# Performance work log

Measured on AMD Instinct MI355X. Metric: run time of the kernel, lower is better.

## Reference

```python
import jax, jax.numpy as jnp
import numpy as np

TOP_K = 2
LORA_SCALE = 32.0 / 16.0  # alpha / rank


def setup_inputs() -> dict:
    key = jax.random.key(0)
    ks = jax.random.split(key, 11)
    N, D, F, E, R = 1024, 2048, 5632, 8, 16
    s = lambda k, shape, fan: jax.random.normal(k, shape, jnp.float32) / np.sqrt(fan)
    return {
        "x": jax.random.normal(ks[0], (N, D), jnp.float32),
        "gate_w": s(ks[1], (E, D), D),
        "W1": s(ks[2], (F, D), D),
        "W3": s(ks[3], (F, D), D),
        "W2": s(ks[4], (D, F), F),
        "A1": s(ks[5], (E, R, D), D),
        "B1": s(ks[6], (F, R), R)[None].repeat(E, 0) * 0.0 + s(ks[6], (E, F, R), R),
        "A3": s(ks[7], (E, R, D), D),
        "B3": s(ks[8], (E, F, R), R),
        "A2": s(ks[9], (E, R, F), F),
        "B2": s(ks[10], (E, D, R), R),
    }


def reference(x, gate_w, W1, W3, W2, A1, B1, A3, B3, A2, B2):
    # --- router: softmax over experts, top-k, renormalized combine weights ---
    logits = x @ gate_w.T                                   # [N, E]
    probs = jax.nn.softmax(logits, axis=-1)
    topw, topi = jax.lax.top_k(probs, TOP_K)                # [N, K]
    topw = topw / jnp.sum(topw, axis=-1, keepdims=True)
    E = gate_w.shape[0]
    w = jnp.sum(jax.nn.one_hot(topi, E, dtype=x.dtype) * topw[..., None], axis=1)  # [N, E]

    # --- experts: shared base weights + per-expert LoRA (fused SwiGLU) ---
    base1 = x @ W1.T                                        # [N, F]
    base3 = x @ W3.T                                        # [N, F]
    l1 = jnp.einsum("nd,erd->ner", x, A1)                   # rank-R bottleneck
    l3 = jnp.einsum("nd,erd->ner", x, A3)
    h1 = base1[:, None, :] + LORA_SCALE * jnp.einsum("ner,efr->nef", l1, B1)  # [N, E, F]
    h3 = base3[:, None, :] + LORA_SCALE * jnp.einsum("ner,efr->nef", l3, B3)
    s = jax.nn.silu(h1) * h3                                # [N, E, F]

    # down-projection: shared W2 applied to the routed mixture, plus per-expert LoRA
    s_mix = jnp.einsum("ne,nef->nf", w, s)                  # [N, F]
    out = s_mix @ W2.T                                      # [N, D]
    l2 = jnp.einsum("nef,erf->ner", s, A2) * (w[:, :, None] * LORA_SCALE)
    out = out + jnp.einsum("ner,edr->nd", l2, B2)           # [N, D]
    return out, logits
```

## Files before the change

kernel.cpp:

```cpp
#include <hip/hip_runtime.h>

typedef unsigned int u32;
typedef unsigned short u16;

#define N_TOK 1024
#define D_DIM 2048
#define F_DIM 5632
#define E_NUM 8
#define R_DIM 16
#define LSCALE 2.0f
#define FT 256
#define NT (F_DIM / FT)
#define TC 8
#define BN13 11520
#define ZSPLIT 8

typedef __bf16 bf16x8 __attribute__((ext_vector_type(8)));
typedef float f32x4 __attribute__((ext_vector_type(4)));
typedef u16 u16x8 __attribute__((ext_vector_type(8)));

__device__ inline u16 f2bf(float f) {
    u32 u = __builtin_bit_cast(u32, f);
    u32 r = (u + 0x7fffu + ((u >> 16) & 1u)) >> 16;
    return (u16)r;
}
__device__ inline float bf2f(u16 h) {
    u32 u = ((u32)h) << 16;
    return __builtin_bit_cast(float, u);
}

#define LGKM0() do { asm volatile("s_waitcnt lgkmcnt(0)" ::: "memory"); \
                     __builtin_amdgcn_sched_barrier(0); } while (0)
#define VMC(n)  do { asm volatile("s_waitcnt vmcnt(" #n ")" ::: "memory"); \
                     __builtin_amdgcn_sched_barrier(0); } while (0)

__global__ __launch_bounds__(256) void cvt_all(const float* __restrict__ x,
                                               const float* __restrict__ W1,
                                               const float* __restrict__ W3,
                                               const float* __restrict__ A1,
                                               const float* __restrict__ A3,
                                               const float* __restrict__ W2,
                                               const float* __restrict__ B1,
                                               const float* __restrict__ B3,
                                               u16* __restrict__ xb,
                                               u16* __restrict__ w13,
                                               u16* __restrict__ w2b,
                                               u16* __restrict__ b1b,
                                               u16* __restrict__ b3b) {
    int i = blockIdx.x * 256 + threadIdx.x;
    const float* src;
    u16* dst;
    int off;
    if (i < 524288)       { src = x;  dst = xb;             off = i; }
    else if (i < 3407872) { src = W1; dst = w13;            off = i - 524288; }
    else if (i < 6291456) { src = W3; dst = w13 + 11534336; off = i - 3407872; }
    else if (i < 6356992) { src = A1; dst = w13 + 23068672; off = i - 6291456; }
    else if (i < 6422528) { src = A3; dst = w13 + 23330816; off = i - 6356992; }
    else if (i < 9306112) { src = W2; dst = w2b;            off = i - 6422528; }
    else if (i < 9486336) { src = B1; dst = b1b;            off = i - 9306112; }
    else                  { src = B3; dst = b3b;            off = i - 9486336; }
    float4 v = ((const float4*)src)[off];
    union { u16 h[4]; ushort4 u4; } o;
    o.h[0] = f2bf(v.x); o.h[1] = f2bf(v.y); o.h[2] = f2bf(v.z); o.h[3] = f2bf(v.w);
    ((ushort4*)dst)[off] = o.u4;
}

__global__ __launch_bounds__(256) void a2_transpose(const float* __restrict__ A2,
                                                    u16* __restrict__ A2t) {
    int e = blockIdx.y;
    int f = blockIdx.x * 256 + threadIdx.x;
    u16 row[16];
#pragma unroll
    for (int r = 0; r < 16; ++r)
        row[r] = f2bf(A2[((size_t)e * R_DIM + r) * F_DIM + f]);
    u16* dst = A2t + ((size_t)e * F_DIM + f) * 16;
#pragma unroll
    for (int q = 0; q < 2; ++q)
        ((ulonglong2*)dst)[q] = ((ulonglong2*)row)[q];
}

__global__ __launch_bounds__(256) void router_kernel(const float* __restrict__ x,
                                                     const float* __restrict__ gw,
                                                     float* __restrict__ logits,
                                                     int* __restrict__ ridx,
                                                     float* __restrict__ rw) {
    int n = blockIdx.x;
    int tid = threadIdx.x;
    float part[E_NUM];
#pragma unroll
    for (int e = 0; e < E_NUM; ++e) part[e] = 0.f;
    const float* xr = x + (size_t)n * D_DIM;
    for (int d = tid; d < D_DIM; d += 256) {
        float xv = xr[d];
#pragma unroll
        for (int e = 0; e < E_NUM; ++e) part[e] += xv * gw[e * D_DIM + d];
    }
    __shared__ float sh[E_NUM][256];
#pragma unroll
    for (int e = 0; e < E_NUM; ++e) sh[e][tid] = part[e];
    __syncthreads();
    for (int off = 128; off > 0; off >>= 1) {
        if (tid < off) {
#pragma unroll
            for (int e = 0; e < E_NUM; ++e) sh[e][tid] += sh[e][tid + off];
        }
        __syncthreads();
    }
    if (tid == 0) {
        float lg[E_NUM], p[E_NUM];
        float mx = -1e30f;
        for (int e = 0; e < E_NUM; ++e) {
            lg[e] = sh[e][0];
            logits[n * E_NUM + e] = lg[e];
            if (lg[e] > mx) mx = lg[e];
        }
        float s = 0.f;
        for (int e = 0; e < E_NUM; ++e) { p[e] = expf(lg[e] - mx); s += p[e]; }
        for (int e = 0; e < E_NUM; ++e) p[e] /= s;
        int i1 = 0;
        for (int e = 1; e < E_NUM; ++e) if (p[e] > p[i1]) i1 = e;
        int i2 = (i1 == 0) ? 1 : 0;
        for (int e = 0; e < E_NUM; ++e) if (e != i1 && p[e] > p[i2]) i2 = e;
        float t = p[i1] + p[i2];
        ridx[n * 2] = i1; ridx[n * 2 + 1] = i2;
        rw[n * 2] = p[i1] / t; rw[n * 2 + 1] = p[i2] / t;
    }
}

__global__ __launch_bounds__(64) void zero_counts(int* counts) {
    if (threadIdx.x < E_NUM) counts[threadIdx.x] = 0;
}
__global__ __launch_bounds__(256) void build_lists(const int* __restrict__ ridx,
                                                   int* __restrict__ counts,
                                                   u32* __restrict__ lists) {
    int n = blockIdx.x * 256 + threadIdx.x;
    if (n >= N_TOK) return;
#pragma unroll
    for (int k = 0; k < 2; ++k) {
        int e = ridx[n * 2 + k];
        int slot = atomicAdd(&counts[e], 1);
        lists[e * N_TOK + slot] = (u32)n | ((u32)k << 16);
    }
}

__global__ __launch_bounds__(512, 2) void gemm256(const u16* __restrict__ A,
                                                  const u16* __restrict__ B,
                                                  float* __restrict__ C,
                                                  int N, int K, int kslice,
                                                  int mode, int ntm, int ntn) {
    __shared__ __align__(16) u16 lds[2][2][2][256 * 32];

    const int nb = gridDim.x;
    const int fb = blockIdx.x;
    const int qq = nb >> 3, rr = nb & 7;
    const int xcd = fb & 7, lo = fb >> 3;
    const int wg = (xcd < rr ? xcd * (qq + 1) : rr * (qq + 1) + (xcd - rr) * qq) + lo;

    const int mt = wg % ntm;
    const int t2 = wg / ntm;
    const int nt = t2 % ntn;
    const int zt = t2 / ntn;

    const int bm0 = mt * 256;
    const int bn0 = nt * 256;
    const int kb = zt * kslice;

    const int tid = threadIdx.x;
    const int lane = tid & 63;
    const int wave = tid >> 6;
    const int quad = lane >> 4;
    const int l16 = lane & 15;
    const int swz = (l16 & 8) << 1;
    const int wm = (wave >> 2) * 128;
    const int wn = (wave & 3) * 64;

    f32x4 zero = {0.f, 0.f, 0.f, 0.f};
    f32x4 acc[8][4];
#pragma unroll
    for (int i = 0; i < 8; ++i)
#pragma unroll
        for (int j = 0; j < 4; ++j) acc[i][j] = zero;

    auto stageHalf = [&](const u16* __restrict__ G, int mat, int buf, int h,
                         int k0, int rowBase) {
#pragma unroll
        for (int j = 0; j < 2; ++j) {
            int seg = wave * 2 + j;
            int plane = seg >> 3;
            int rb = seg & 7;
            int r = h * 128 + rb * 16 + (lane >> 2);
            int slot = lane & 3;
            int gcol = k0 + plane * 32 + ((slot * 8) ^ ((r & 8) << 1));
            const u16* gp = G + (size_t)(rowBase + r) * K + gcol;
            u16* lp = &lds[mat][buf][plane][(h * 128 + rb * 16) * 32] + lane * 8;
            __builtin_amdgcn_global_load_lds((const __attribute__((address_space(1))) u32*)gp,
                                             (__attribute__((address_space(3))) u32*)lp,
                                             16, 0, 0);
        }
    };

    const int nk = kslice >> 6;

    stageHalf(A, 0, 0, 0, kb, bm0);
    stageHalf(A, 0, 0, 1, kb, bm0);
    stageHalf(B, 1, 0, 0, kb, bn0);
    stageHalf(B, 1, 0, 1, kb, bn0);
    stageHalf(A, 0, 1, 0, kb + 64, bm0);
    stageHalf(A, 0, 1, 1, kb + 64, bm0);
    VMC(4);
    __builtin_amdgcn_s_barrier();

    bf16x8 af[8][2];
    for (int t = 0; t < nk; ++t) {
        const int buf = t & 1;
        const int k0 = kb + t * 64;

        {
            bf16x8 bf[2][2];
#pragma unroll
            for (int mi = 0; mi < 4; ++mi)
#pragma unroll
                for (int ks = 0; ks < 2; ++ks)
                    af[mi][ks] = *(const bf16x8*)&lds[0][buf][ks]
                        [(wm + mi * 16 + l16) * 32 + ((quad * 8) ^ swz)];
#pragma unroll
            for (int ni = 0; ni < 2; ++ni)
#pragma unroll
                for (int ks = 0; ks < 2; ++ks)
                    bf[ni][ks] = *(const bf16x8*)&lds[1][buf][ks]
                        [(wn + ni * 16 + l16) * 32 + ((quad * 8) ^ swz)];
            if (t + 1 < nk) stageHalf(B, 1, buf ^ 1, 0, k0 + 64, bn0);
            __builtin_amdgcn_s_barrier();
            LGKM0();
            __builtin_amdgcn_s_setprio(1);
#pragma unroll
            for (int mi = 0; mi < 4; ++mi)
#pragma unroll
                for (int ni = 0; ni < 2; ++ni)
#pragma unroll
                    for (int ks = 0; ks < 2; ++ks)
                        acc[mi][ni] = __builtin_amdgcn_mfma_f32_16x16x32_bf16(
                            af[mi][ks], bf[ni][ks], acc[mi][ni], 0, 0, 0);
            __builtin_amdgcn_s_setprio(0);
            __builtin_amdgcn_s_barrier();
        }

        {
            bf16x8 bf[2][2];
#pragma unroll
            for (int mi = 0; mi < 4; ++mi)
#pragma unroll
                for (int ks = 0; ks < 2; ++ks)
                    af[4 + mi][ks] = *(const bf16x8*)&lds[0][buf][ks]
                        [(wm + (4 + mi) * 16 + l16) * 32 + ((quad * 8) ^ swz)];
#pragma unroll
            for (int ni = 0; ni < 2; ++ni)
#pragma unroll
                for (int ks = 0; ks < 2; ++ks)
                    bf[ni][ks] = *(const bf16x8*)&lds[1][buf][ks]
                        [(wn + (2 + ni) * 16 + l16) * 32 + ((quad * 8) ^ swz)];
            if (t + 1 < nk) stageHalf(B, 1, buf ^ 1, 1, k0 + 64, bn0);
            __builtin_amdgcn_s_barrier();
            LGKM0();
            __builtin_amdgcn_s_setprio(1);
#pragma unroll
            for (int mi = 0; mi < 4; ++mi)
#pragma unroll
                for (int ni = 0; ni < 2; ++ni)
#pragma unroll
                    for (int ks = 0; ks < 2; ++ks)
                        acc[mi][2 + ni] = __builtin_amdgcn_mfma_f32_16x16x32_bf16(
                            af[mi][ks], bf[ni][ks], acc[mi][2 + ni], 0, 0, 0);
            __builtin_amdgcn_s_setprio(0);
            __builtin_amdgcn_s_barrier();

            if (t + 2 < nk) stageHalf(A, 0, buf, 0, k0 + 128, bm0);
            __builtin_amdgcn_s_barrier();
            __builtin_amdgcn_s_setprio(1);
#pragma unroll
            for (int mi = 0; mi < 4; ++mi)
#pragma unroll
                for (int ni = 0; ni < 2; ++ni)
#pragma unroll
                    for (int ks = 0; ks < 2; ++ks)
                        acc[4 + mi][2 + ni] = __builtin_amdgcn_mfma_f32_16x16x32_bf16(
                            af[4 + mi][ks], bf[ni][ks], acc[4 + mi][2 + ni], 0, 0, 0);
            __builtin_amdgcn_s_setprio(0);
            __builtin_amdgcn_s_barrier();
        }

        {
            bf16x8 bf[2][2];
#pragma unroll
            for (int ni = 0; ni < 2; ++ni)
#pragma unroll
                for (int ks = 0; ks < 2; ++ks)
                    bf[ni][ks] = *(const bf16x8*)&lds[1][buf][ks]
                        [(wn + ni * 16 + l16) * 32 + ((quad * 8) ^ swz)];
            if (t + 2 < nk) stageHalf(A, 0, buf, 1, k0 + 128, bm0);
            __builtin_amdgcn_s_barrier();
            LGKM0();
            __builtin_amdgcn_s_setprio(1);
#pragma unroll
            for (int mi = 0; mi < 4; ++mi)
#pragma unroll
                for (int ni = 0; ni < 2; ++ni)
#pragma unroll
                    for (int ks = 0; ks < 2; ++ks)
                        acc[4 + mi][ni] = __builtin_amdgcn_mfma_f32_16x16x32_bf16(
                            af[4 + mi][ks], bf[ni][ks], acc[4 + mi][ni], 0, 0, 0);
            __builtin_amdgcn_s_setprio(0);
            if (t < nk - 2)       { VMC(4); }
            else if (t == nk - 2) { VMC(0); }
            __builtin_amdgcn_s_barrier();
        }
    }

    float* Cz = C + (size_t)zt * ntm * 256 * N;
#pragma unroll
    for (int mi = 0; mi < 8; ++mi)
#pragma unroll
        for (int ni = 0; ni < 4; ++ni) {
            int col = bn0 + wn + ni * 16 + l16;
#pragma unroll
            for (int i = 0; i < 4; ++i) {
                int row = bm0 + wm + mi * 16 + quad * 4 + i;
                if (mode == 1) {
                    ((u16*)C)[(size_t)row * N + col] = f2bf(acc[mi][ni][i]);
                } else {
                    Cz[(size_t)row * N + col] = acc[mi][ni][i];
                }
            }
        }
}

__global__ __launch_bounds__(256) void act_v2b(const u16* __restrict__ base13,
                                               const u16* __restrict__ B1b,
                                               const u16* __restrict__ B3b,
                                               const u32* __restrict__ lists,
                                               const int* __restrict__ counts,
                                               const float* __restrict__ rw,
                                               u16* __restrict__ sbuf) {
    const int ft = blockIdx.x;
    const int e  = blockIdx.y;
    const int z  = blockIdx.z;
    const int tid = threadIdx.x;
    const int lane = tid & 63;
    const int wave = tid >> 6;
    const int f_lane = ft * FT + lane * 4;

    u16x8 w1c[8], w3c[8];
    {
        const u16* p1 = B1b + ((size_t)e * F_DIM + f_lane) * 16;
        const u16* p3 = B3b + ((size_t)e * F_DIM + f_lane) * 16;
#pragma unroll
        for (int c = 0; c < 8; ++c) {
            w1c[c] = *(const u16x8*)(p1 + c * 8);
            w3c[c] = *(const u16x8*)(p3 + c * 8);
        }
    }

    const int T = counts[e];
    for (int i = z * 4 + wave; i < T; i += TC * 4) {
        u32 ent = lists[e * N_TOK + i];
        int n = (int)(ent & 0xFFFFu);
        int k = (int)(ent >> 16);
        float wt = rw[n * 2 + k];

        float la1[16], la3[16];
        {
            const u16x8* pl1 = (const u16x8*)(base13 + (size_t)n * BN13 + 11264 + e * 16);
            const u16x8* pl3 = (const u16x8*)(base13 + (size_t)n * BN13 + 11392 + e * 16);
#pragma unroll
            for (int h = 0; h < 2; ++h) {
                u16x8 t1 = pl1[h], t3 = pl3[h];
#pragma unroll
                for (int qq = 0; qq < 8; ++qq) {
                    la1[h * 8 + qq] = LSCALE * bf2f(t1[qq]);
                    la3[h * 8 + qq] = LSCALE * bf2f(t3[qq]);
                }
            }
        }

        ushort4 b1u = *(const ushort4*)(base13 + (size_t)n * BN13 + f_lane);
        ushort4 b3u = *(const ushort4*)(base13 + (size_t)n * BN13 + 5632 + f_lane);
        const u16* b1p = (const u16*)&b1u;
        const u16* b3p = (const u16*)&b3u;

        u16 sv[4];
#pragma unroll
        for (int j = 0; j < 4; ++j) {
            float h1 = bf2f(b1p[j]);
            float h3 = bf2f(b3p[j]);
#pragma unroll
            for (int qq = 0; qq < 8; ++qq) {
                h1 += la1[qq] * bf2f(w1c[2 * j][qq]);
                h3 += la3[qq] * bf2f(w3c[2 * j][qq]);
            }
#pragma unroll
            for (int qq = 0; qq < 8; ++qq) {
                h1 += la1[8 + qq] * bf2f(w1c[2 * j + 1][qq]);
                h3 += la3[8 + qq] * bf2f(w3c[2 * j + 1][qq]);
            }
            float sg = h1 / (1.f + __expf(-h1));
            sv[j] = f2bf(wt * sg * h3);
        }
        *(ushort4*)(sbuf + ((size_t)k * N_TOK + n) * F_DIM + f_lane) = *(ushort4*)sv;
    }
}

__global__ __launch_bounds__(256) void combine_kernel(const u16* __restrict__ sbuf,
                                                      u16* __restrict__ smix) {
    size_t i = ((size_t)blockIdx.x * 256 + threadIdx.x) * 8;
    u16x8 a = *(const u16x8*)(sbuf + i);
    u16x8 b = *(const u16x8*)(sbuf + (size_t)N_TOK * F_DIM + i);
    u16x8 o;
#pragma unroll
    for (int q = 0; q < 8; ++q) o[q] = f2bf(bf2f(a[q]) + bf2f(b[q]));
    *(u16x8*)(smix + i) = o;
}

__global__ __launch_bounds__(256) void lora_down_v4(const u16* __restrict__ sbuf,
                                                    const u16* __restrict__ A2t,
                                                    const int* __restrict__ ridx,
                                                    const float* __restrict__ B2,
                                                    const float* __restrict__ pbuf,
                                                    float* __restrict__ out) {
    const int n = blockIdx.x, tid = threadIdx.x;
    __shared__ float part[2][32][16];
    __shared__ float fin[2][16];
    __shared__ int se[2];
    if (tid < 2) se[tid] = ridx[n * 2 + tid];
    __syncthreads();

    {
        const int k = tid >> 7;
        const int tt = tid & 127;
        const int rq = tt & 3;
        const int fc = tt >> 2;
        const int e = se[k];
        const u16* srow = sbuf + ((size_t)k * N_TOK + n) * F_DIM + fc * 176;
        const u16* arow = A2t + ((size_t)e * F_DIM + fc * 176) * 16 + rq * 4;
        float acc0 = 0.f, acc1 = 0.f, acc2 = 0.f, acc3 = 0.f;
#pragma unroll 4
        for (int f = 0; f < 176; ++f) {
            float sv = bf2f(srow[f]);
            ushort4 wr = *(const ushort4*)(arow + (size_t)f * 16);
            acc0 += sv * bf2f(wr.x);
            acc1 += sv * bf2f(wr.y);
            acc2 += sv * bf2f(wr.z);
            acc3 += sv * bf2f(wr.w);
        }
        part[k][fc][rq * 4 + 0] = acc0;
        part[k][fc][rq * 4 + 1] = acc1;
        part[k][fc][rq * 4 + 2] = acc2;
        part[k][fc][rq * 4 + 3] = acc3;
    }
    __syncthreads();
    if (tid < 32) {
        int k = tid >> 4, r = tid & 15;
        float s = 0.f;
#pragma unroll
        for (int fc = 0; fc < 32; ++fc) s += part[k][fc][r];
        fin[k][r] = LSCALE * s;
    }
    __syncthreads();

    float a0[16], a1v[16];
#pragma unroll
    for (int r = 0; r < 16; ++r) { a0[r] = fin[0][r]; a1v[r] = fin[1][r]; }
    const float* B2a = B2 + (size_t)se[0] * D_DIM * R_DIM;
    const float* B2b = B2 + (size_t)se[1] * D_DIM * R_DIM;
    const float* prow = pbuf + (size_t)n * D_DIM;
    float* orow = out + (size_t)n * D_DIM;
    for (int d = tid; d < D_DIM; d += 256) {
        const float4* pa = (const float4*)(B2a + (size_t)d * 16);
        const float4* pb = (const float4*)(B2b + (size_t)d * 16);
        float acc = 0.f;
#pragma unroll
        for (int q = 0; q < 4; ++q) {
            float4 va = pa[q];
            acc += a0[q * 4] * va.x + a0[q * 4 + 1] * va.y +
                   a0[q * 4 + 2] * va.z + a0[q * 4 + 3] * va.w;
            float4 vb = pb[q];
            acc += a1v[q * 4] * vb.x + a1v[q * 4 + 1] * vb.y +
                   a1v[q * 4 + 2] * vb.z + a1v[q * 4 + 3] * vb.w;
        }
        float ps = 0.f;
#pragma unroll
        for (int z = 0; z < ZSPLIT; ++z)
            ps += prow[(size_t)z * N_TOK * D_DIM + d];
        orow[d] = acc + ps;
    }
}

extern "C" void kernel_launch(void* const* d_in, const int* in_sizes, int n_in,
                              void* d_out, int out_size, void* d_ws, size_t ws_size,
                              hipStream_t stream) {
    const float* x  = (const float*)d_in[0];
    const float* gw = (const float*)d_in[1];
    const float* W1 = (const float*)d_in[2];
    const float* W3 = (const float*)d_in[3];
    const float* W2 = (const float*)d_in[4];
    const float* A1 = (const float*)d_in[5];
    const float* B1 = (const float*)d_in[6];
    const float* A3 = (const float*)d_in[7];
    const float* B3 = (const float*)d_in[8];
    const float* A2 = (const float*)d_in[9];
    const float* B2 = (const float*)d_in[10];
    float* out = (float*)d_out;
    float* logits = out + (size_t)N_TOK * D_DIM;

    char* ws = (char*)d_ws;
    size_t off = 0;
    auto alloc = [&](size_t bytes) { char* p = ws + off; off += (bytes + 255) & ~(size_t)255; return p; };
    u16*   xb    = (u16*)alloc((size_t)N_TOK * D_DIM * 2);
    u16*   W13b  = (u16*)alloc((size_t)BN13 * D_DIM * 2);
    u16*   W2b   = (u16*)alloc((size_t)D_DIM * F_DIM * 2);
    u16*   base13= (u16*)alloc((size_t)N_TOK * BN13 * 2);
    int*   ridx  = (int*)alloc((size_t)N_TOK * 2 * 4);
    float* rwt   = (float*)alloc((size_t)N_TOK * 2 * 4);
    u16*   B1b   = (u16*)alloc((size_t)E_NUM * F_DIM * R_DIM * 2);
    u16*   B3b   = (u16*)alloc((size_t)E_NUM * F_DIM * R_DIM * 2);
    u16*   A2t   = (u16*)alloc((size_t)E_NUM * F_DIM * R_DIM * 2);
    int*   counts= (int*)alloc(64);
    u32*   lists = (u32*)alloc((size_t)E_NUM * N_TOK * 4);
    u16*   sbuf  = (u16*)alloc((size_t)2 * N_TOK * F_DIM * 2);
    u16*   smixb = (u16*)alloc((size_t)N_TOK * F_DIM * 2);
    float* pbuf  = (float*)alloc((size_t)ZSPLIT * N_TOK * D_DIM * 4);
    (void)ws_size; (void)in_sizes; (void)n_in; (void)out_size;

    cvt_all<<<37760, 256, 0, stream>>>(x, W1, W3, A1, A3, W2, B1, B3,
                                       xb, W13b, W2b, B1b, B3b);
    a2_transpose<<<dim3(F_DIM / 256, E_NUM), 256, 0, stream>>>(A2, A2t);

    router_kernel<<<N_TOK, 256, 0, stream>>>(x, gw, logits, ridx, rwt);
    zero_counts<<<1, 64, 0, stream>>>(counts);
    build_lists<<<N_TOK / 256, 256, 0, stream>>>(ridx, counts, lists);

    gemm256<<<180, 512, 0, stream>>>(xb, W13b, (float*)base13,
                                     BN13, D_DIM, D_DIM, 1, 4, 45);

    act_v2b<<<dim3(NT, E_NUM, TC), 256, 0, stream>>>(base13, B1b, B3b,
                                                     lists, counts, rwt, sbuf);

    combine_kernel<<<(N_TOK * F_DIM / 8) / 256, 256, 0, stream>>>(sbuf, smixb);

    gemm256<<<256, 512, 0, stream>>>(smixb, W2b, pbuf,
                                     D_DIM, F_DIM, 704, 0, 4, 8);

    lora_down_v4<<<N_TOK, 256, 0, stream>>>(sbuf, A2t, ridx, B2, pbuf, out);
}
```

Before: 404.5 us.

## Restructure GEMM main loop into four k-split phases with B prefetched two ahead

Reorganizes the inner MFMA loop of the tiled GEMM from three phases (mixed quadrants, both k-halves) into four phases. Each phase covers half of the M rows and one 32-wide k-slice against all N columns. The staging schedule is swapped so B is double-buffered two tiles ahead and A one tile ahead. Register footprint drops because fragments are held per k-slice (4 A + 8 B vectors) instead of af[8][2]. Each phase now issues 16 MFMAs with a barrier between phases, and the prefetch ordering and barrier placement change how global-to-LDS loads overlap with compute.

```diff
diff --git a/kernel.cpp b/kernel.cpp
--- a/kernel.cpp
+++ b/kernel.cpp
@@ -199,116 +199,103 @@
         }
     };
 
+    auto ldA = [&](int buf, int ks, int mi) -> bf16x8 {
+        return *(const bf16x8*)&lds[0][buf][ks]
+            [(wm + mi * 16 + l16) * 32 + ((quad * 8) ^ swz)];
+    };
+    auto ldB = [&](int buf, int ks, int ni) -> bf16x8 {
+        return *(const bf16x8*)&lds[1][buf][ks]
+            [(wn + ni * 16 + l16) * 32 + ((quad * 8) ^ swz)];
+    };
+
     const int nk = kslice >> 6;
 
     stageHalf(A, 0, 0, 0, kb, bm0);
     stageHalf(A, 0, 0, 1, kb, bm0);
     stageHalf(B, 1, 0, 0, kb, bn0);
     stageHalf(B, 1, 0, 1, kb, bn0);
-    stageHalf(A, 0, 1, 0, kb + 64, bm0);
-    stageHalf(A, 0, 1, 1, kb + 64, bm0);
+    stageHalf(B, 1, 1, 0, kb + 64, bn0);
+    stageHalf(B, 1, 1, 1, kb + 64, bn0);
     VMC(4);
     __builtin_amdgcn_s_barrier();
 
-    bf16x8 af[8][2];
     for (int t = 0; t < nk; ++t) {
         const int buf = t & 1;
         const int k0 = kb + t * 64;
+        bf16x8 bq0[4], bq1[4];
 
         {
-            bf16x8 bf[2][2];
-#pragma unroll
-            for (int mi = 0; mi < 4; ++mi)
-#pragma unroll
-                for (int ks = 0; ks < 2; ++ks)
-                    af[mi][ks] = *(const bf16x8*)&lds[0][buf][ks]
-                        [(wm + mi * 16 + l16) * 32 + ((quad * 8) ^ swz)];
-#pragma unroll
-            for (int ni = 0; ni < 2; ++ni)
-#pragma unroll
-                for (int ks = 0; ks < 2; ++ks)
-                    bf[ni][ks] = *(const bf16x8*)&lds[1][buf][ks]
-                        [(wn + ni * 16 + l16) * 32 + ((quad * 8) ^ swz)];
-            if (t + 1 < nk) stageHalf(B, 1, buf ^ 1, 0, k0 + 64, bn0);
+            bf16x8 av[4];
+#pragma unroll
+            for (int mi = 0; mi < 4; ++mi) av[mi] = ldA(buf, 0, mi);
+#pragma unroll
+            for (int ni = 0; ni < 4; ++ni) bq0[ni] = ldB(buf, 0, ni);
+            if (t + 1 < nk) stageHalf(A, 0, buf ^ 1, 0, k0 + 64, bm0);
             __builtin_amdgcn_s_barrier();
             LGKM0();
             __builtin_amdgcn_s_setprio(1);
 #pragma unroll
             for (int mi = 0; mi < 4; ++mi)
 #pragma unroll
-                for (int ni = 0; ni < 2; ++ni)
-#pragma unroll
-                    for (int ks = 0; ks < 2; ++ks)
-                        acc[mi][ni] = __builtin_amdgcn_mfma_f32_16x16x32_bf16(
-                            af[mi][ks], bf[ni][ks], acc[mi][ni], 0, 0, 0);
+                for (int ni = 0; ni < 4; ++ni)
+                    acc[mi][ni] = __builtin_amdgcn_mfma_f32_16x16x32_bf16(
+                        av[mi], bq0[ni], acc[mi][ni], 0, 0, 0);
             __builtin_amdgcn_s_setprio(0);
             __builtin_amdgcn_s_barrier();
         }
 
         {
-            bf16x8 bf[2][2];
-#pragma unroll
-            for (int mi = 0; mi < 4; ++mi)
-#pragma unroll
-                for (int ks = 0; ks < 2; ++ks)
-                    af[4 + mi][ks] = *(const bf16x8*)&lds[0][buf][ks]
-                        [(wm + (4 + mi) * 16 + l16) * 32 + ((quad * 8) ^ swz)];
-#pragma unroll
-            for (int ni = 0; ni < 2; ++ni)
-#pragma unroll
-                for (int ks = 0; ks < 2; ++ks)
-                    bf[ni][ks] = *(const bf16x8*)&lds[1][buf][ks]
-                        [(wn + (2 + ni) * 16 + l16) * 32 + ((quad * 8) ^ swz)];
-            if (t + 1 < nk) stageHalf(B, 1, buf ^ 1, 1, k0 + 64, bn0);
+            bf16x8 av[4];
+#pragma unroll
+            for (int mi = 0; mi < 4; ++mi) av[mi] = ldA(buf, 0, 4 + mi);
+#pragma unroll
+            for (int ni = 0; ni < 4; ++ni) bq1[ni] = ldB(buf, 1, ni);
+            if (t + 1 < nk) stageHalf(A, 0, buf ^ 1, 1, k0 + 64, bm0);
             __builtin_amdgcn_s_barrier();
             LGKM0();
             __builtin_amdgcn_s_setprio(1);
 #pragma unroll
             for (int mi = 0; mi < 4; ++mi)
 #pragma unroll
-                for (int ni = 0; ni < 2; ++ni)
-#pragma unroll
-                    for (int ks = 0; ks < 2; ++ks)
-                        acc[mi][2 + ni] = __builtin_amdgcn_mfma_f32_16x16x32_bf16(
-                            af[mi][ks], bf[ni][ks], acc[mi][2 + ni], 0, 0, 0);
+                for (int ni = 0; ni < 4; ++ni)
+                    acc[4 + mi][ni] = __builtin_amdgcn_mfma_f32_16x16x32_bf16(
+                        av[mi], bq0[ni], acc[4 + mi][ni], 0, 0, 0);
             __builtin_amdgcn_s_setprio(0);
             __builtin_amdgcn_s_barrier();
-
-            if (t + 2 < nk) stageHalf(A, 0, buf, 0, k0 + 128, bm0);
-            __builtin_amdgcn_s_barrier();
-            __builtin_amdgcn_s_setprio(1);
-#pragma unroll
-            for (int mi = 0; mi < 4; ++mi)
-#pragma unroll
-                for (int ni = 0; ni < 2; ++ni)
-#pragma unroll
-                    for (int ks = 0; ks < 2; ++ks)
-                        acc[4 + mi][2 + ni] = __builtin_amdgcn_mfma_f32_16x16x32_bf16(
-                            af[4 + mi][ks], bf[ni][ks], acc[4 + mi][2 + ni], 0, 0, 0);
-            __builtin_amdgcn_s_setprio(0);
-            __builtin_amdgcn_s_barrier();
         }
 
         {
-            bf16x8 bf[2][2];
-#pragma unroll
-            for (int ni = 0; ni < 2; ++ni)
-#pragma unroll
-                for (int ks = 0; ks < 2; ++ks)
-                    bf[ni][ks] = *(const bf16x8*)&lds[1][buf][ks]
-                        [(wn + ni * 16 + l16) * 32 + ((quad * 8) ^ swz)];
-            if (t + 2 < nk) stageHalf(A, 0, buf, 1, k0 + 128, bm0);
+            bf16x8 av[4];
+#pragma unroll
+            for (int mi = 0; mi < 4; ++mi) av[mi] = ldA(buf, 1, mi);
+            if (t + 2 < nk) stageHalf(B, 1, buf, 0, k0 + 128, bn0);
             __builtin_amdgcn_s_barrier();
             LGKM0();
             __builtin_amdgcn_s_setprio(1);
 #pragma unroll
             for (int mi = 0; mi < 4; ++mi)
 #pragma unroll
-                for (int ni = 0; ni < 2; ++ni)
-#pragma unroll
-                    for (int ks = 0; ks < 2; ++ks)
-                        acc[4 + mi][ni] = __builtin_amdgcn_mfma_f32_16x16x32_bf16(
-                            af[4 + mi][ks], bf[ni][ks], acc[4 + mi][ni], 0, 0, 0);
+                for (int ni = 0; ni < 4; ++ni)
+                    acc[mi][ni] = __builtin_amdgcn_mfma_f32_16x16x32_bf16(
+                        av[mi], bq1[ni], acc[mi][ni], 0, 0, 0);
+            __builtin_amdgcn_s_setprio(0);
+            __builtin_amdgcn_s_barrier();
+        }
+
+        {
+            bf16x8 av[4];
+#pragma unroll
+            for (int mi = 0; mi < 4; ++mi) av[mi] = ldA(buf, 1, 4 + mi);
+            if (t + 2 < nk) stageHalf(B, 1, buf, 1, k0 + 128, bn0);
+            __builtin_amdgcn_s_barrier();
+            LGKM0();
+            __builtin_amdgcn_s_setprio(1);
+#pragma unroll
+            for (int mi = 0; mi < 4; ++mi)
+#pragma unroll
+                for (int ni = 0; ni < 4; ++ni)
+                    acc[4 + mi][ni] = __builtin_amdgcn_mfma_f32_16x16x32_bf16(
+                        av[mi], bq1[ni], acc[4 + mi][ni], 0, 0, 0);
             __builtin_amdgcn_s_setprio(0);
             if (t < nk - 2)       { VMC(4); }
             else if (t == nk - 2) { VMC(0); }
```

After: 401.7 us. No clear change (-0.7%).
